# Kernel optimization log

Hardware: AMD Instinct MI355X
Metric: run time of the kernel (lower is better)

## Reference

```python
import jax, jax.numpy as jnp
import numpy as np

N = 10000        # num nodes
E = 160000       # num edges (before self-loops)
D = 128          # input_dim == 4*hidden_dim
H = 4            # heads for first 19 layers
C = 32           # hidden_dim (per-head channels)
L_MID = 19       # layers with relu (convs[0..18]); last layer is heads=1, concat=False
NEG_SLOPE = 0.2  # PyG GATConv default negative_slope
EPS = 1e-16      # PyG softmax epsilon


def setup_inputs() -> dict:
    key = jax.random.key(0)
    ks = jax.random.split(key, 10)
    s = 0.1  # keep activations stable across 20 layers
    x = jax.random.normal(ks[0], (N, D), jnp.float32)
    edge_index = jax.random.randint(ks[1], (2, E), 0, N, dtype=jnp.int64)
    Ws = jax.random.normal(ks[2], (L_MID, D, H * C), jnp.float32) * s
    a_src = jax.random.normal(ks[3], (L_MID, H, C), jnp.float32) * s
    a_dst = jax.random.normal(ks[4], (L_MID, H, C), jnp.float32) * s
    bs = jnp.zeros((L_MID, H * C), jnp.float32)
    W_last = jax.random.normal(ks[5], (D, D), jnp.float32) * s
    a_src_last = jax.random.normal(ks[6], (1, D), jnp.float32) * s
    a_dst_last = jax.random.normal(ks[7], (1, D), jnp.float32) * s
    b_last = jnp.zeros((D,), jnp.float32)
    return {"x": x, "edge_index": edge_index, "Ws": Ws, "a_src": a_src,
            "a_dst": a_dst, "bs": bs, "W_last": W_last,
            "a_src_last": a_src_last, "a_dst_last": a_dst_last, "b_last": b_last}


def _gat_layer(x, src, dst, W, asrc, adst, heads, ch):
    # x: [N, Din]; W: [Din, heads*ch]; asrc/adst: [heads, ch]
    h = (x @ W).reshape(N, heads, ch)                       # [N,H,C]
    es = jnp.einsum('nhc,hc->nh', h, asrc)                  # [N,H]
    ed = jnp.einsum('nhc,hc->nh', h, adst)                  # [N,H]
    e = jax.nn.leaky_relu(es[src] + ed[dst], NEG_SLOPE)     # [Etot,H]
    # segment softmax over incoming edges of each dst node
    m = jax.ops.segment_max(e, dst, num_segments=N)         # [N,H]
    p = jnp.exp(e - m[dst])
    z = jax.ops.segment_sum(p, dst, num_segments=N)         # [N,H]
    alpha = p / (z[dst] + EPS)                              # [Etot,H]
    msg = h[src] * alpha[:, :, None]                        # [Etot,H,C]
    return jax.ops.segment_sum(msg, dst, num_segments=N)    # [N,H,C]


def reference(x, edge_index, Ws, a_src, a_dst, bs, W_last, a_src_last, a_dst_last, b_last):
    # PyG GATConv adds self-loops by default
    loop = jnp.arange(N, dtype=edge_index.dtype)
    src = jnp.concatenate([edge_index[0], loop])
    dst = jnp.concatenate([edge_index[1], loop])

    def mid_step(h, params):
        W, asrc, adst, b = params
        out = _gat_layer(h, src, dst, W, asrc, adst, H, C).reshape(N, H * C) + b
        return jax.nn.relu(out), None  # training dropout omitted (eval mode)

    x, _ = jax.lax.scan(mid_step, x, (Ws, a_src, a_dst, bs))
    # final layer: heads=1, concat=False -> mean over heads, no relu
    out = _gat_layer(x, src, dst, W_last, a_src_last, a_dst_last, 1, D)
    return out.mean(axis=1) + b_last
```

## Files before the change

kernel.cpp:

```cpp
#include <hip/hip_runtime.h>
#include <hip/hip_bf16.h>
#include <math.h>

#define D 128
#define NEG 0.2f
#define EPSV 1e-16f
#define NPB 8
#define GRP_N 4

__global__ void scan_kernel(const int* __restrict__ deg, int N, int* __restrict__ row_ptr, int* __restrict__ cursor){
  __shared__ int part[1024];
  const int CH = 16;
  int t = threadIdx.x;
  int base = t*CH;
  int local[CH]; int s = 0;
  #pragma unroll
  for (int j=0;j<CH;j++){ int idx=base+j; int v = (idx<N)? deg[idx] : 0; local[j]=s; s+=v; }
  part[t]=s; __syncthreads();
  for (int off=1; off<1024; off<<=1){
    int v = (t>=off)? part[t-off] : 0;
    __syncthreads();
    part[t]+=v;
    __syncthreads();
  }
  int cb = (t==0)? 0 : part[t-1];
  #pragma unroll
  for (int j=0;j<CH;j++){ int idx=base+j; if(idx<N){ int r=cb+local[j]; row_ptr[idx]=r; cursor[idx]=r; } }
  if (t==1023) row_ptr[N]=part[1023];
}

__global__ void scatter_kernel(const int* __restrict__ esrc, const int* __restrict__ edst,
                               int E, int N, int* __restrict__ cursor, int* __restrict__ csr_src){
  int i = blockIdx.x*blockDim.x + threadIdx.x;
  int tot = E + N;
  if (i>=tot) return;
  int s, d2;
  if (i<E){ s=esrc[i]; d2=edst[i]; } else { s=i-E; d2=i-E; }
  int pos = atomicAdd(&cursor[d2],1);
  csr_src[pos]=s;
}

template<int HNEXT>
__device__ __forceinline__ void gemv_phase(const float (*rbuf)[D], int nbase, int N,
                                           const float* __restrict__ Wn,
                                           const float* __restrict__ av_, const float* __restrict__ bv_,
                                           float* __restrict__ h_out, float* __restrict__ es_out,
                                           float* __restrict__ ed_out, float (*pE)[2], float (*pD)[2]){
  const int t   = threadIdx.x;
  const int col = t & (D-1);
  const int g   = t >> 7;
  const float av = av_[col], bv = bv_[col];
  const float* __restrict__ r[GRP_N];
  #pragma unroll
  for (int j=0;j<GRP_N;j++) r[j] = rbuf[g*GRP_N + j];
  float acc[GRP_N];
  #pragma unroll
  for (int j=0;j<GRP_N;j++) acc[j]=0.f;

  #pragma unroll 4
  for (int k=0;k<D;k+=4){
    const float w0 = Wn[(size_t)(k+0)*D + col];
    const float w1 = Wn[(size_t)(k+1)*D + col];
    const float w2 = Wn[(size_t)(k+2)*D + col];
    const float w3 = Wn[(size_t)(k+3)*D + col];
    #pragma unroll
    for (int j=0;j<GRP_N;j++){
      const float4 xv = *reinterpret_cast<const float4*>(r[j] + k);
      acc[j] = fmaf(xv.w, w3, fmaf(xv.z, w2, fmaf(xv.y, w1, fmaf(xv.x, w0, acc[j]))));
    }
  }

  if constexpr (HNEXT==4){
    #pragma unroll
    for (int j=0;j<GRP_N;j++){
      const int n = nbase + g*GRP_N + j;
      if (n < N){
        __builtin_nontemporal_store(acc[j], &h_out[(size_t)n*D + col]);
        float ps = acc[j]*av, pd = acc[j]*bv;
        #pragma unroll
        for (int off=16; off; off>>=1){ ps += __shfl_xor(ps, off, 32); pd += __shfl_xor(pd, off, 32); }
        if ((col&31)==0){ es_out[n*4 + (col>>5)] = ps; ed_out[n*4 + (col>>5)] = pd; }
      }
    }
  } else {
    const int half = (t>>6)&1;
    #pragma unroll
    for (int j=0;j<GRP_N;j++){
      const int n = nbase + g*GRP_N + j;
      float ps = 0.f, pd = 0.f;
      if (n < N){
        __builtin_nontemporal_store(acc[j], &h_out[(size_t)n*D + col]);
        ps = acc[j]*av; pd = acc[j]*bv;
      }
      #pragma unroll
      for (int off=32; off; off>>=1){ ps += __shfl_xor(ps, off, 64); pd += __shfl_xor(pd, off, 64); }
      if ((t&63)==0){ pE[g*GRP_N+j][half]=ps; pD[g*GRP_N+j][half]=pd; }
    }
    __syncthreads();
    if (t < NPB){
      const int n = nbase + t;
      if (n < N){
        es_out[n] = pE[t][0]+pE[t][1];
        ed_out[n] = pD[t][0]+pD[t][1];
      }
    }
  }
}

__launch_bounds__(256, 4)
__global__ void linear0_kernel(const float* __restrict__ x, const float* __restrict__ Wn,
                               const float* __restrict__ an_src, const float* __restrict__ an_dst,
                               int N, int E, const int* __restrict__ edst, int* __restrict__ deg,
                               float* __restrict__ h_out, float* __restrict__ es_out, float* __restrict__ ed_out){
  __shared__ float rbuf[NPB][D];
  __shared__ float pE[NPB][2], pD[NPB][2];
  const int t = threadIdx.x;
  const int nbase = blockIdx.x*NPB;
  {
    const int gid = blockIdx.x*256 + t;
    const int gs  = gridDim.x*256;
    const int tot = E + N;
    for (int i = gid; i < tot; i += gs){
      const int d2 = (i < E) ? edst[i] : (i - E);
      atomicAdd(&deg[d2], 1);
    }
  }
  {
    const int row = t >> 5;
    const int cc  = (t & 31) * 4;
    int n = nbase + row; if (n > N-1) n = N-1;
    const float4 v = *reinterpret_cast<const float4*>(x + (size_t)n*D + cc);
    *reinterpret_cast<float4*>(&rbuf[row][cc]) = v;
  }
  __syncthreads();
  gemv_phase<4>(rbuf, nbase, N, Wn, an_src, an_dst, h_out, es_out, ed_out, pE, pD);
}

template<int HNEXT>
__launch_bounds__(256, 4)
__global__ void fused_kernel(const float* __restrict__ h, const float* __restrict__ es, const float* __restrict__ ed,
                             const int* __restrict__ row_ptr, const int* __restrict__ csr_src,
                             const float* __restrict__ bias,
                             const float* __restrict__ Wn, const float* __restrict__ an_src, const float* __restrict__ an_dst,
                             int N, float* __restrict__ h_out, float* __restrict__ es_out, float* __restrict__ ed_out){
  __shared__ int   sIdx[NPB][32];
  __shared__ float sP[NPB][32][4];
  __shared__ float rbuf[NPB][D];
  __shared__ float pE[NPB][2], pD[NPB][2];
  const int t = threadIdx.x;
  const int hw  = t >> 5;
  const int l32 = t & 31;
  const int cq   = l32 * 4;
  const int myh4 = l32 >> 3;
  const int nbase = blockIdx.x*NPB;
  const int n = nbase + hw;

  if (n < N){
    const int start = row_ptr[n], end = row_ptr[n+1];
    const float4 edv = *reinterpret_cast<const float4*>(ed + (size_t)n*4);
    float4 acc = make_float4(0.f,0.f,0.f,0.f);
    float z = 0.f;

    for (int t0 = start; t0 < end; t0 += 32){
      const int cnt = min(32, end - t0);
      {
        int sOff = 0; float p0=0.f,p1=0.f,p2=0.f,p3=0.f;
        if (l32 < cnt){
          const int s = csr_src[t0 + l32];
          sOff = s*D;
          const float4 e4 = *reinterpret_cast<const float4*>(es + (size_t)s*4);
          float q0 = e4.x + edv.x; q0 = (q0>=0.f)? q0 : NEG*q0; q0 = fminf(q0, 80.f);
          float q1 = e4.y + edv.y; q1 = (q1>=0.f)? q1 : NEG*q1; q1 = fminf(q1, 80.f);
          float q2 = e4.z + edv.z; q2 = (q2>=0.f)? q2 : NEG*q2; q2 = fminf(q2, 80.f);
          float q3 = e4.w + edv.w; q3 = (q3>=0.f)? q3 : NEG*q3; q3 = fminf(q3, 80.f);
          p0 = __expf(q0); p1 = __expf(q1); p2 = __expf(q2); p3 = __expf(q3);
        }
        sIdx[hw][l32] = sOff;
        *reinterpret_cast<float4*>(&sP[hw][l32][0]) = make_float4(p0,p1,p2,p3);
      }
      #pragma unroll 8
      for (int e = 0; e < cnt; e++){
        const int   off = sIdx[hw][e];
        const float p   = sP[hw][e][myh4];
        const float4 hv = *reinterpret_cast<const float4*>(h + (size_t)off + cq);
        z += p;
        acc.x = fmaf(p, hv.x, acc.x);
        acc.y = fmaf(p, hv.y, acc.y);
        acc.z = fmaf(p, hv.z, acc.z);
        acc.w = fmaf(p, hv.w, acc.w);
      }
    }
    const float inv = 1.f/(z + EPSV);
    const float4 bv = *reinterpret_cast<const float4*>(bias + cq);
    float4 o;
    o.x = fmaxf(fmaf(acc.x, inv, bv.x), 0.f);
    o.y = fmaxf(fmaf(acc.y, inv, bv.y), 0.f);
    o.z = fmaxf(fmaf(acc.z, inv, bv.z), 0.f);
    o.w = fmaxf(fmaf(acc.w, inv, bv.w), 0.f);
    *reinterpret_cast<float4*>(&rbuf[hw][cq]) = o;
  } else {
    *reinterpret_cast<float4*>(&rbuf[hw][cq]) = make_float4(0.f,0.f,0.f,0.f);
  }
  __syncthreads();
  gemv_phase<HNEXT>(rbuf, nbase, N, Wn, an_src, an_dst, h_out, es_out, ed_out, pE, pD);
}

__launch_bounds__(256, 4)
__global__ void final_agg_kernel(const float* __restrict__ h, const float* __restrict__ es, const float* __restrict__ ed,
                                 const int* __restrict__ row_ptr, const int* __restrict__ csr_src,
                                 const float* __restrict__ bias, float* __restrict__ out, int N){
  __shared__ int   sIdx[NPB][32];
  __shared__ float sP[NPB][32];
  const int t = threadIdx.x;
  const int hw  = t >> 5;
  const int l32 = t & 31;
  const int cq  = l32 * 4;
  const int n = blockIdx.x*NPB + hw;
  if (n >= N) return;
  const int start = row_ptr[n], end = row_ptr[n+1];
  const float edn = ed[n];
  float4 acc = make_float4(0.f,0.f,0.f,0.f);
  float z = 0.f;
  for (int t0 = start; t0 < end; t0 += 32){
    const int cnt = min(32, end - t0);
    {
      int sOff = 0; float p0 = 0.f;
      if (l32 < cnt){
        const int s = csr_src[t0 + l32];
        sOff = s*D;
        float q0 = es[s] + edn; q0 = (q0>=0.f)? q0 : NEG*q0; q0 = fminf(q0, 80.f);
        p0 = __expf(q0);
      }
      sIdx[hw][l32] = sOff;
      sP[hw][l32] = p0;
    }
    #pragma unroll 8
    for (int e = 0; e < cnt; e++){
      const int   off = sIdx[hw][e];
      const float p   = sP[hw][e];
      const float4 hv = *reinterpret_cast<const float4*>(h + (size_t)off + cq);
      z += p;
      acc.x = fmaf(p, hv.x, acc.x);
      acc.y = fmaf(p, hv.y, acc.y);
      acc.z = fmaf(p, hv.z, acc.z);
      acc.w = fmaf(p, hv.w, acc.w);
    }
  }
  const float inv = 1.f/(z + EPSV);
  const float4 bv = *reinterpret_cast<const float4*>(bias + cq);
  float4 o;
  o.x = fmaf(acc.x, inv, bv.x);
  o.y = fmaf(acc.y, inv, bv.y);
  o.z = fmaf(acc.z, inv, bv.z);
  o.w = fmaf(acc.w, inv, bv.w);
  *reinterpret_cast<float4*>(&out[(size_t)n*D + cq]) = o;
}

extern "C" void kernel_launch(void* const* d_in, const int* in_sizes, int n_in,
                              void* d_out, int out_size, void* d_ws, size_t ws_size,
                              hipStream_t stream) {
  const float* x          = (const float*)d_in[0];
  const int*   ei         = (const int*)d_in[1];
  const float* Ws         = (const float*)d_in[2];
  const float* a_src      = (const float*)d_in[3];
  const float* a_dst      = (const float*)d_in[4];
  const float* bs         = (const float*)d_in[5];
  const float* W_last     = (const float*)d_in[6];
  const float* a_src_last = (const float*)d_in[7];
  const float* a_dst_last = (const float*)d_in[8];
  const float* b_last     = (const float*)d_in[9];

  const int N = in_sizes[0]/D;
  const int E = in_sizes[1]/2;
  const int L = in_sizes[2]/(D*D);
  const int* esrc = ei;
  const int* edst = ei + E;

  char* ws = (char*)d_ws;
  float* h0  = (float*)ws;  ws += (size_t)N*D*sizeof(float);
  float* h1  = (float*)ws;  ws += (size_t)N*D*sizeof(float);
  float* es0 = (float*)ws;  ws += (size_t)N*4*sizeof(float);
  float* es1 = (float*)ws;  ws += (size_t)N*4*sizeof(float);
  float* ed0 = (float*)ws;  ws += (size_t)N*4*sizeof(float);
  float* ed1 = (float*)ws;  ws += (size_t)N*4*sizeof(float);
  int* deg     = (int*)ws;  ws += (size_t)N*sizeof(int);
  int* row_ptr = (int*)ws;  ws += (size_t)(N+1)*sizeof(int);
  int* cursor  = (int*)ws;  ws += (size_t)N*sizeof(int);
  int* csr_src = (int*)ws;  ws += (size_t)(E+N)*sizeof(int);

  const int tot = E + N;
  const int gA = (N + NPB - 1)/NPB;

  hipMemsetAsync(deg, 0, (size_t)N*sizeof(int), stream);
  linear0_kernel<<<gA, 256, 0, stream>>>(x, Ws, a_src, a_dst, N, E, edst, deg, h0, es0, ed0);
  scan_kernel<<<1, 1024, 0, stream>>>(deg, N, row_ptr, cursor);
  scatter_kernel<<<(tot+255)/256, 256, 0, stream>>>(esrc, edst, E, N, cursor, csr_src);

  const float *hc = h0, *esc = es0, *edc = ed0;
  float *hn = h1, *esn = es1, *edn = ed1;

  for (int l = 0; l < L-1; l++){
    fused_kernel<4><<<gA, 256, 0, stream>>>(hc, esc, edc, row_ptr, csr_src,
                                            bs + (size_t)l*D,
                                            Ws + (size_t)(l+1)*D*D, a_src + (size_t)(l+1)*D, a_dst + (size_t)(l+1)*D,
                                            N, hn, esn, edn);
    const float* tf;
    tf = hc;  hc = hn;  hn = (float*)tf;
    tf = esc; esc = esn; esn = (float*)tf;
    tf = edc; edc = edn; edn = (float*)tf;
  }

  fused_kernel<1><<<gA, 256, 0, stream>>>(hc, esc, edc, row_ptr, csr_src,
                                          bs + (size_t)(L-1)*D,
                                          W_last, a_src_last, a_dst_last,
                                          N, hn, esn, edn);
  {
    const float* tf;
    tf = hc;  hc = hn;  hn = (float*)tf;
    tf = esc; esc = esn; esn = (float*)tf;
    tf = edc; edc = edn; edn = (float*)tf;
  }

  final_agg_kernel<<<gA, 256, 0, stream>>>(hc, esc, edc, row_ptr, csr_src, b_last, (float*)d_out, N);
}
```

Baseline: 433.4 us.

## Fuse all GAT layers into one persistent kernel with grid-wide barriers

Replaces the per-layer kernel launches (20 fused layers plus final aggregation) with a single persistent kernel of 500 blocks × 512 threads, each owning 20 nodes. A hand-rolled slotted atomic grid barrier separates layers. Cross-block data now goes through relaxed agent-scope atomic loads and stores, split into float2 pieces. The degree count moves back into its own kernel. This aims to remove launch overhead and tail gaps between layers, but it relies on every block being co-resident, since the barrier has a timeout escape. It also gives up vectorized float4 and nontemporal memory accesses.

```diff
diff --git a/kernel.cpp b/kernel.cpp
--- a/kernel.cpp
+++ b/kernel.cpp
@@ -5,8 +5,50 @@
 #define D 128
 #define NEG 0.2f
 #define EPSV 1e-16f
-#define NPB 8
-#define GRP_N 4
+#define NPB 20
+#define GRPN 5
+#define NSYNC 20
+#define BAR_U32 144
+
+__device__ __forceinline__ float2 ld_sys_f2(const float* p){
+  unsigned long long u = __hip_atomic_load((const unsigned long long*)p, __ATOMIC_RELAXED, __HIP_MEMORY_SCOPE_AGENT);
+  float2 f; f.x = __uint_as_float((unsigned)u); f.y = __uint_as_float((unsigned)(u >> 32));
+  return f;
+}
+__device__ __forceinline__ float ld_sys_f1(const float* p){
+  return __uint_as_float(__hip_atomic_load((const unsigned*)p, __ATOMIC_RELAXED, __HIP_MEMORY_SCOPE_AGENT));
+}
+__device__ __forceinline__ void st_sys_f1(float* p, float v){
+  __hip_atomic_store((unsigned*)p, __float_as_uint(v), __ATOMIC_RELAXED, __HIP_MEMORY_SCOPE_AGENT);
+}
+
+__device__ __forceinline__ void gsync(unsigned* bar, int idx){
+  __syncthreads();
+  if (threadIdx.x == 0){
+    unsigned* b = bar + idx * BAR_U32;
+    const unsigned g = gridDim.x;
+    const unsigned nslots = (g < 8u) ? g : 8u;
+    const unsigned slot = blockIdx.x & 7u;
+    const unsigned target = ((g - 1u - slot) >> 3) + 1u;
+    const unsigned a = __hip_atomic_fetch_add(b + slot*16, 1u, __ATOMIC_RELAXED, __HIP_MEMORY_SCOPE_AGENT);
+    if (a == target - 1u)
+      __hip_atomic_fetch_add(b + 128, 1u, __ATOMIC_RELAXED, __HIP_MEMORY_SCOPE_AGENT);
+    int fuse = 0;
+    while (__hip_atomic_load(b + 128, __ATOMIC_RELAXED, __HIP_MEMORY_SCOPE_AGENT) < nslots){
+      __builtin_amdgcn_s_sleep(2);
+      if (++fuse > (1<<22)) break;
+    }
+  }
+  __syncthreads();
+}
+
+__global__ void count_kernel(const int* __restrict__ edst, int E, int N, int* __restrict__ deg){
+  int i = blockIdx.x*blockDim.x + threadIdx.x;
+  int tot = E + N;
+  if (i >= tot) return;
+  int d = (i < E) ? edst[i] : (i - E);
+  atomicAdd(&deg[d], 1);
+}
 
 __global__ void scan_kernel(const int* __restrict__ deg, int N, int* __restrict__ row_ptr, int* __restrict__ cursor){
   __shared__ int part[1024];
@@ -44,18 +86,18 @@
 __device__ __forceinline__ void gemv_phase(const float (*rbuf)[D], int nbase, int N,
                                            const float* __restrict__ Wn,
                                            const float* __restrict__ av_, const float* __restrict__ bv_,
-                                           float* __restrict__ h_out, float* __restrict__ es_out,
-                                           float* __restrict__ ed_out, float (*pE)[2], float (*pD)[2]){
+                                           float* h_out, float* es_out, float* ed_out,
+                                           float (*pE)[2], float (*pD)[2]){
   const int t   = threadIdx.x;
   const int col = t & (D-1);
   const int g   = t >> 7;
   const float av = av_[col], bv = bv_[col];
-  const float* __restrict__ r[GRP_N];
+  const float* __restrict__ r[GRPN];
   #pragma unroll
-  for (int j=0;j<GRP_N;j++) r[j] = rbuf[g*GRP_N + j];
-  float acc[GRP_N];
+  for (int j=0;j<GRPN;j++) r[j] = rbuf[g*GRPN + j];
+  float acc[GRPN];
   #pragma unroll
-  for (int j=0;j<GRP_N;j++) acc[j]=0.f;
+  for (int j=0;j<GRPN;j++) acc[j]=0.f;
 
   #pragma unroll 4
   for (int k=0;k<D;k+=4){
@@ -64,7 +106,7 @@
     const float w2 = Wn[(size_t)(k+2)*D + col];
     const float w3 = Wn[(size_t)(k+3)*D + col];
     #pragma unroll
-    for (int j=0;j<GRP_N;j++){
+    for (int j=0;j<GRPN;j++){
       const float4 xv = *reinterpret_cast<const float4*>(r[j] + k);
       acc[j] = fmaf(xv.w, w3, fmaf(xv.z, w2, fmaf(xv.y, w1, fmaf(xv.x, w0, acc[j]))));
     }
@@ -72,95 +114,57 @@
 
   if constexpr (HNEXT==4){
     #pragma unroll
-    for (int j=0;j<GRP_N;j++){
-      const int n = nbase + g*GRP_N + j;
+    for (int j=0;j<GRPN;j++){
+      const int n = nbase + g*GRPN + j;
       if (n < N){
-        __builtin_nontemporal_store(acc[j], &h_out[(size_t)n*D + col]);
+        st_sys_f1(&h_out[(size_t)n*D + col], acc[j]);
         float ps = acc[j]*av, pd = acc[j]*bv;
         #pragma unroll
         for (int off=16; off; off>>=1){ ps += __shfl_xor(ps, off, 32); pd += __shfl_xor(pd, off, 32); }
-        if ((col&31)==0){ es_out[n*4 + (col>>5)] = ps; ed_out[n*4 + (col>>5)] = pd; }
+        if ((col&31)==0){ st_sys_f1(&es_out[n*4 + (col>>5)], ps); st_sys_f1(&ed_out[n*4 + (col>>5)], pd); }
       }
     }
   } else {
     const int half = (t>>6)&1;
     #pragma unroll
-    for (int j=0;j<GRP_N;j++){
-      const int n = nbase + g*GRP_N + j;
+    for (int j=0;j<GRPN;j++){
+      const int n = nbase + g*GRPN + j;
       float ps = 0.f, pd = 0.f;
       if (n < N){
-        __builtin_nontemporal_store(acc[j], &h_out[(size_t)n*D + col]);
+        st_sys_f1(&h_out[(size_t)n*D + col], acc[j]);
         ps = acc[j]*av; pd = acc[j]*bv;
       }
       #pragma unroll
       for (int off=32; off; off>>=1){ ps += __shfl_xor(ps, off, 64); pd += __shfl_xor(pd, off, 64); }
-      if ((t&63)==0){ pE[g*GRP_N+j][half]=ps; pD[g*GRP_N+j][half]=pd; }
+      if ((t&63)==0){ pE[g*GRPN+j][half]=ps; pD[g*GRPN+j][half]=pd; }
     }
     __syncthreads();
     if (t < NPB){
       const int n = nbase + t;
       if (n < N){
-        es_out[n] = pE[t][0]+pE[t][1];
-        ed_out[n] = pD[t][0]+pD[t][1];
-      }
-    }
-  }
-}
-
-__launch_bounds__(256, 4)
-__global__ void linear0_kernel(const float* __restrict__ x, const float* __restrict__ Wn,
-                               const float* __restrict__ an_src, const float* __restrict__ an_dst,
-                               int N, int E, const int* __restrict__ edst, int* __restrict__ deg,
-                               float* __restrict__ h_out, float* __restrict__ es_out, float* __restrict__ ed_out){
-  __shared__ float rbuf[NPB][D];
-  __shared__ float pE[NPB][2], pD[NPB][2];
+        st_sys_f1(&es_out[n], pE[t][0]+pE[t][1]);
+        st_sys_f1(&ed_out[n], pD[t][0]+pD[t][1]);
+      }
+    }
+  }
+}
+
+__device__ __forceinline__ void mid_agg(const float* h, const float* es, const float* ed,
+                                        const int* __restrict__ row_ptr, const int* __restrict__ csr_src,
+                                        const float* __restrict__ bias,
+                                        float (*rbuf)[D], int (*sIdx)[32], float (*sP)[32][4],
+                                        int nbase, int N){
   const int t = threadIdx.x;
-  const int nbase = blockIdx.x*NPB;
-  {
-    const int gid = blockIdx.x*256 + t;
-    const int gs  = gridDim.x*256;
-    const int tot = E + N;
-    for (int i = gid; i < tot; i += gs){
-      const int d2 = (i < E) ? edst[i] : (i - E);
-      atomicAdd(&deg[d2], 1);
-    }
-  }
-  {
-    const int row = t >> 5;
-    const int cc  = (t & 31) * 4;
-    int n = nbase + row; if (n > N-1) n = N-1;
-    const float4 v = *reinterpret_cast<const float4*>(x + (size_t)n*D + cc);
-    *reinterpret_cast<float4*>(&rbuf[row][cc]) = v;
-  }
-  __syncthreads();
-  gemv_phase<4>(rbuf, nbase, N, Wn, an_src, an_dst, h_out, es_out, ed_out, pE, pD);
-}
-
-template<int HNEXT>
-__launch_bounds__(256, 4)
-__global__ void fused_kernel(const float* __restrict__ h, const float* __restrict__ es, const float* __restrict__ ed,
-                             const int* __restrict__ row_ptr, const int* __restrict__ csr_src,
-                             const float* __restrict__ bias,
-                             const float* __restrict__ Wn, const float* __restrict__ an_src, const float* __restrict__ an_dst,
-                             int N, float* __restrict__ h_out, float* __restrict__ es_out, float* __restrict__ ed_out){
-  __shared__ int   sIdx[NPB][32];
-  __shared__ float sP[NPB][32][4];
-  __shared__ float rbuf[NPB][D];
-  __shared__ float pE[NPB][2], pD[NPB][2];
-  const int t = threadIdx.x;
-  const int hw  = t >> 5;
-  const int l32 = t & 31;
-  const int cq   = l32 * 4;
-  const int myh4 = l32 >> 3;
-  const int nbase = blockIdx.x*NPB;
-  const int n = nbase + hw;
-
-  if (n < N){
+  const int hw = t >> 5, l32 = t & 31;
+  const int cq = l32*4, myh4 = l32>>3;
+  for (int local = hw; local < NPB; local += 16){
+    const int n = nbase + local;
+    if (n >= N){ *reinterpret_cast<float4*>(&rbuf[local][cq]) = make_float4(0.f,0.f,0.f,0.f); continue; }
     const int start = row_ptr[n], end = row_ptr[n+1];
-    const float4 edv = *reinterpret_cast<const float4*>(ed + (size_t)n*4);
+    const float2 edA = ld_sys_f2(ed + (size_t)n*4);
+    const float2 edB = ld_sys_f2(ed + (size_t)n*4 + 2);
     float4 acc = make_float4(0.f,0.f,0.f,0.f);
     float z = 0.f;
-
     for (int t0 = start; t0 < end; t0 += 32){
       const int cnt = min(32, end - t0);
       {
@@ -168,11 +172,12 @@
         if (l32 < cnt){
           const int s = csr_src[t0 + l32];
           sOff = s*D;
-          const float4 e4 = *reinterpret_cast<const float4*>(es + (size_t)s*4);
-          float q0 = e4.x + edv.x; q0 = (q0>=0.f)? q0 : NEG*q0; q0 = fminf(q0, 80.f);
-          float q1 = e4.y + edv.y; q1 = (q1>=0.f)? q1 : NEG*q1; q1 = fminf(q1, 80.f);
-          float q2 = e4.z + edv.z; q2 = (q2>=0.f)? q2 : NEG*q2; q2 = fminf(q2, 80.f);
-          float q3 = e4.w + edv.w; q3 = (q3>=0.f)? q3 : NEG*q3; q3 = fminf(q3, 80.f);
+          const float2 eA = ld_sys_f2(es + (size_t)s*4);
+          const float2 eB = ld_sys_f2(es + (size_t)s*4 + 2);
+          float q0 = eA.x + edA.x; q0 = (q0>=0.f)? q0 : NEG*q0; q0 = fminf(q0, 80.f);
+          float q1 = eA.y + edA.y; q1 = (q1>=0.f)? q1 : NEG*q1; q1 = fminf(q1, 80.f);
+          float q2 = eB.x + edB.x; q2 = (q2>=0.f)? q2 : NEG*q2; q2 = fminf(q2, 80.f);
+          float q3 = eB.y + edB.y; q3 = (q3>=0.f)? q3 : NEG*q3; q3 = fminf(q3, 80.f);
           p0 = __expf(q0); p1 = __expf(q1); p2 = __expf(q2); p3 = __expf(q3);
         }
         sIdx[hw][l32] = sOff;
@@ -182,12 +187,13 @@
       for (int e = 0; e < cnt; e++){
         const int   off = sIdx[hw][e];
         const float p   = sP[hw][e][myh4];
-        const float4 hv = *reinterpret_cast<const float4*>(h + (size_t)off + cq);
+        const float2 hA = ld_sys_f2(h + (size_t)off + cq);
+        const float2 hB = ld_sys_f2(h + (size_t)off + cq + 2);
         z += p;
-        acc.x = fmaf(p, hv.x, acc.x);
-        acc.y = fmaf(p, hv.y, acc.y);
-        acc.z = fmaf(p, hv.z, acc.z);
-        acc.w = fmaf(p, hv.w, acc.w);
+        acc.x = fmaf(p, hA.x, acc.x);
+        acc.y = fmaf(p, hA.y, acc.y);
+        acc.z = fmaf(p, hB.x, acc.z);
+        acc.w = fmaf(p, hB.y, acc.w);
       }
     }
     const float inv = 1.f/(z + EPSV);
@@ -197,63 +203,115 @@
     o.y = fmaxf(fmaf(acc.y, inv, bv.y), 0.f);
     o.z = fmaxf(fmaf(acc.z, inv, bv.z), 0.f);
     o.w = fmaxf(fmaf(acc.w, inv, bv.w), 0.f);
-    *reinterpret_cast<float4*>(&rbuf[hw][cq]) = o;
-  } else {
-    *reinterpret_cast<float4*>(&rbuf[hw][cq]) = make_float4(0.f,0.f,0.f,0.f);
+    *reinterpret_cast<float4*>(&rbuf[local][cq]) = o;
+  }
+}
+
+__device__ __forceinline__ void final_agg(const float* h, const float* es, const float* ed,
+                                          const int* __restrict__ row_ptr, const int* __restrict__ csr_src,
+                                          const float* __restrict__ bias, float* __restrict__ out,
+                                          int (*sIdx)[32], float (*sP)[32][4], int nbase, int N){
+  const int t = threadIdx.x;
+  const int hw = t >> 5, l32 = t & 31;
+  const int cq = l32*4;
+  for (int local = hw; local < NPB; local += 16){
+    const int n = nbase + local;
+    if (n >= N) continue;
+    const int start = row_ptr[n], end = row_ptr[n+1];
+    const float edn = ld_sys_f1(ed + n);
+    float4 acc = make_float4(0.f,0.f,0.f,0.f);
+    float z = 0.f;
+    for (int t0 = start; t0 < end; t0 += 32){
+      const int cnt = min(32, end - t0);
+      {
+        int sOff = 0; float p0 = 0.f;
+        if (l32 < cnt){
+          const int s = csr_src[t0 + l32];
+          sOff = s*D;
+          float q0 = ld_sys_f1(es + s) + edn; q0 = (q0>=0.f)? q0 : NEG*q0; q0 = fminf(q0, 80.f);
+          p0 = __expf(q0);
+        }
+        sIdx[hw][l32] = sOff;
+        sP[hw][l32][0] = p0;
+      }
+      #pragma unroll 8
+      for (int e = 0; e < cnt; e++){
+        const int   off = sIdx[hw][e];
+        const float p   = sP[hw][e][0];
+        const float2 hA = ld_sys_f2(h + (size_t)off + cq);
+        const float2 hB = ld_sys_f2(h + (size_t)off + cq + 2);
+        z += p;
+        acc.x = fmaf(p, hA.x, acc.x);
+        acc.y = fmaf(p, hA.y, acc.y);
+        acc.z = fmaf(p, hB.x, acc.z);
+        acc.w = fmaf(p, hB.y, acc.w);
+      }
+    }
+    const float inv = 1.f/(z + EPSV);
+    const float4 bv = *reinterpret_cast<const float4*>(bias + cq);
+    float4 o;
+    o.x = fmaf(acc.x, inv, bv.x);
+    o.y = fmaf(acc.y, inv, bv.y);
+    o.z = fmaf(acc.z, inv, bv.z);
+    o.w = fmaf(acc.w, inv, bv.w);
+    *reinterpret_cast<float4*>(&out[(size_t)n*D + cq]) = o;
+  }
+}
+
+__global__ __launch_bounds__(512, 4)
+void gat_persist(const float* __restrict__ x,
+                 const int* __restrict__ row_ptr, const int* __restrict__ csr_src,
+                 const float* __restrict__ Ws, const float* __restrict__ a_src, const float* __restrict__ a_dst,
+                 const float* __restrict__ bs, const float* __restrict__ W_last,
+                 const float* __restrict__ a_src_last, const float* __restrict__ a_dst_last,
+                 const float* __restrict__ b_last,
+                 int N, int L,
+                 float* h0, float* h1, float* es0, float* es1, float* ed0, float* ed1,
+                 unsigned* bar, float* out){
+  __shared__ float rbuf[NPB][D];
+  __shared__ int   sIdx[16][32];
+  __shared__ float sP[16][32][4];
+  __shared__ float pE[NPB][2], pD[NPB][2];
+  const int t = threadIdx.x;
+  const int nbase = blockIdx.x * NPB;
+  int sync_idx = 0;
+
+  for (int i = t; i < NPB*(D/4); i += 512){
+    const int row = i >> 5;
+    const int cc  = (i & 31) * 4;
+    int n = nbase + row; if (n > N-1) n = N-1;
+    *reinterpret_cast<float4*>(&rbuf[row][cc]) = *reinterpret_cast<const float4*>(x + (size_t)n*D + cc);
   }
   __syncthreads();
-  gemv_phase<HNEXT>(rbuf, nbase, N, Wn, an_src, an_dst, h_out, es_out, ed_out, pE, pD);
-}
-
-__launch_bounds__(256, 4)
-__global__ void final_agg_kernel(const float* __restrict__ h, const float* __restrict__ es, const float* __restrict__ ed,
-                                 const int* __restrict__ row_ptr, const int* __restrict__ csr_src,
-                                 const float* __restrict__ bias, float* __restrict__ out, int N){
-  __shared__ int   sIdx[NPB][32];
-  __shared__ float sP[NPB][32];
-  const int t = threadIdx.x;
-  const int hw  = t >> 5;
-  const int l32 = t & 31;
-  const int cq  = l32 * 4;
-  const int n = blockIdx.x*NPB + hw;
-  if (n >= N) return;
-  const int start = row_ptr[n], end = row_ptr[n+1];
-  const float edn = ed[n];
-  float4 acc = make_float4(0.f,0.f,0.f,0.f);
-  float z = 0.f;
-  for (int t0 = start; t0 < end; t0 += 32){
-    const int cnt = min(32, end - t0);
-    {
-      int sOff = 0; float p0 = 0.f;
-      if (l32 < cnt){
-        const int s = csr_src[t0 + l32];
-        sOff = s*D;
-        float q0 = es[s] + edn; q0 = (q0>=0.f)? q0 : NEG*q0; q0 = fminf(q0, 80.f);
-        p0 = __expf(q0);
-      }
-      sIdx[hw][l32] = sOff;
-      sP[hw][l32] = p0;
-    }
-    #pragma unroll 8
-    for (int e = 0; e < cnt; e++){
-      const int   off = sIdx[hw][e];
-      const float p   = sP[hw][e];
-      const float4 hv = *reinterpret_cast<const float4*>(h + (size_t)off + cq);
-      z += p;
-      acc.x = fmaf(p, hv.x, acc.x);
-      acc.y = fmaf(p, hv.y, acc.y);
-      acc.z = fmaf(p, hv.z, acc.z);
-      acc.w = fmaf(p, hv.w, acc.w);
-    }
-  }
-  const float inv = 1.f/(z + EPSV);
-  const float4 bv = *reinterpret_cast<const float4*>(bias + cq);
-  float4 o;
-  o.x = fmaf(acc.x, inv, bv.x);
-  o.y = fmaf(acc.y, inv, bv.y);
-  o.z = fmaf(acc.z, inv, bv.z);
-  o.w = fmaf(acc.w, inv, bv.w);
-  *reinterpret_cast<float4*>(&out[(size_t)n*D + cq]) = o;
+  float *hc = h0, *esc = es0, *edc = ed0;
+  float *hn = h1, *esn = es1, *edn = ed1;
+  gemv_phase<4>(rbuf, nbase, N, Ws, a_src, a_dst, hc, esc, edc, pE, pD);
+  gsync(bar, sync_idx++);
+
+  for (int l = 0; l < L-1; ++l){
+    mid_agg(hc, esc, edc, row_ptr, csr_src, bs + (size_t)l*D, rbuf, sIdx, sP, nbase, N);
+    __syncthreads();
+    gemv_phase<4>(rbuf, nbase, N, Ws + (size_t)(l+1)*D*D, a_src + (size_t)(l+1)*D, a_dst + (size_t)(l+1)*D,
+                  hn, esn, edn, pE, pD);
+    gsync(bar, sync_idx++);
+    float* tp;
+    tp = hc;  hc = hn;  hn = tp;
+    tp = esc; esc = esn; esn = tp;
+    tp = edc; edc = edn; edn = tp;
+  }
+
+  mid_agg(hc, esc, edc, row_ptr, csr_src, bs + (size_t)(L-1)*D, rbuf, sIdx, sP, nbase, N);
+  __syncthreads();
+  gemv_phase<1>(rbuf, nbase, N, W_last, a_src_last, a_dst_last, hn, esn, edn, pE, pD);
+  gsync(bar, sync_idx++);
+  {
+    float* tp;
+    tp = hc;  hc = hn;  hn = tp;
+    tp = esc; esc = esn; esn = tp;
+    tp = edc; edc = edn; edn = tp;
+  }
+
+  final_agg(hc, esc, edc, row_ptr, csr_src, b_last, out, sIdx, sP, nbase, N);
 }
 
 extern "C" void kernel_launch(void* const* d_in, const int* in_sizes, int n_in,
@@ -277,49 +335,30 @@
   const int* edst = ei + E;
 
   char* ws = (char*)d_ws;
+  int* deg       = (int*)ws;      ws += (size_t)N*sizeof(int);
+  unsigned* bar  = (unsigned*)ws; ws += (size_t)NSYNC*BAR_U32*sizeof(unsigned);
+  int* row_ptr = (int*)ws;  ws += (size_t)(N+1)*sizeof(int);
+  int* cursor  = (int*)ws;  ws += (size_t)N*sizeof(int);
+  int* csr_src = (int*)ws;  ws += (size_t)(E+N)*sizeof(int);
   float* h0  = (float*)ws;  ws += (size_t)N*D*sizeof(float);
   float* h1  = (float*)ws;  ws += (size_t)N*D*sizeof(float);
   float* es0 = (float*)ws;  ws += (size_t)N*4*sizeof(float);
   float* es1 = (float*)ws;  ws += (size_t)N*4*sizeof(float);
   float* ed0 = (float*)ws;  ws += (size_t)N*4*sizeof(float);
   float* ed1 = (float*)ws;  ws += (size_t)N*4*sizeof(float);
-  int* deg     = (int*)ws;  ws += (size_t)N*sizeof(int);
-  int* row_ptr = (int*)ws;  ws += (size_t)(N+1)*sizeof(int);
-  int* cursor  = (int*)ws;  ws += (size_t)N*sizeof(int);
-  int* csr_src = (int*)ws;  ws += (size_t)(E+N)*sizeof(int);
 
   const int tot = E + N;
   const int gA = (N + NPB - 1)/NPB;
 
-  hipMemsetAsync(deg, 0, (size_t)N*sizeof(int), stream);
-  linear0_kernel<<<gA, 256, 0, stream>>>(x, Ws, a_src, a_dst, N, E, edst, deg, h0, es0, ed0);
+  hipMemsetAsync(deg, 0, (size_t)N*sizeof(int) + (size_t)NSYNC*BAR_U32*sizeof(unsigned), stream);
+  count_kernel<<<(tot+255)/256, 256, 0, stream>>>(edst, E, N, deg);
   scan_kernel<<<1, 1024, 0, stream>>>(deg, N, row_ptr, cursor);
   scatter_kernel<<<(tot+255)/256, 256, 0, stream>>>(esrc, edst, E, N, cursor, csr_src);
 
-  const float *hc = h0, *esc = es0, *edc = ed0;
-  float *hn = h1, *esn = es1, *edn = ed1;
-
-  for (int l = 0; l < L-1; l++){
-    fused_kernel<4><<<gA, 256, 0, stream>>>(hc, esc, edc, row_ptr, csr_src,
-                                            bs + (size_t)l*D,
-                                            Ws + (size_t)(l+1)*D*D, a_src + (size_t)(l+1)*D, a_dst + (size_t)(l+1)*D,
-                                            N, hn, esn, edn);
-    const float* tf;
-    tf = hc;  hc = hn;  hn = (float*)tf;
-    tf = esc; esc = esn; esn = (float*)tf;
-    tf = edc; edc = edn; edn = (float*)tf;
-  }
-
-  fused_kernel<1><<<gA, 256, 0, stream>>>(hc, esc, edc, row_ptr, csr_src,
-                                          bs + (size_t)(L-1)*D,
-                                          W_last, a_src_last, a_dst_last,
-                                          N, hn, esn, edn);
-  {
-    const float* tf;
-    tf = hc;  hc = hn;  hn = (float*)tf;
-    tf = esc; esc = esn; esn = (float*)tf;
-    tf = edc; edc = edn; edn = (float*)tf;
-  }
-
-  final_agg_kernel<<<gA, 256, 0, stream>>>(hc, esc, edc, row_ptr, csr_src, b_last, (float*)d_out, N);
-}
+  gat_persist<<<gA, 512, 0, stream>>>(x, row_ptr, csr_src,
+                                      Ws, a_src, a_dst, bs,
+                                      W_last, a_src_last, a_dst_last, b_last,
+                                      N, L,
+                                      h0, h1, es0, es1, ed0, ed1,
+                                      bar, (float*)d_out);
+}
```

Result: slower. 619.8 us (+43.0%).

## Fold degree count into single-block CSR prep and scatter into linear0

Applied to the files above, without the earlier changes.

Degree counting moves into a single-block kernel that histograms in shared memory and scans it. The CSR scatter moves into linear0, which removes the memset and the separate scatter launch. The aggregation loop is also unrolled by two with dual accumulators to expose more memory-level parallelism. The single block does all 160k atomics serially on one CU, which could cost more than the removed launches. Shared memory is capped at MAXN nodes.

```diff
diff --git a/kernel.cpp b/kernel.cpp
--- a/kernel.cpp
+++ b/kernel.cpp
@@ -7,37 +7,34 @@
 #define EPSV 1e-16f
 #define NPB 8
 #define GRP_N 4
-
-__global__ void scan_kernel(const int* __restrict__ deg, int N, int* __restrict__ row_ptr, int* __restrict__ cursor){
+#define MAXN 10240
+
+__global__ __launch_bounds__(1024, 1)
+void csrprep_kernel(const int* __restrict__ edst, int E, int N,
+                    int* __restrict__ row_ptr, int* __restrict__ cursor){
+  __shared__ int ldeg[MAXN];
   __shared__ int part[1024];
-  const int CH = 16;
-  int t = threadIdx.x;
-  int base = t*CH;
+  const int t = threadIdx.x;
+  for (int i = t; i < N; i += 1024) ldeg[i] = 0;
+  __syncthreads();
+  for (int i = t; i < E; i += 1024) atomicAdd(&ldeg[edst[i]], 1);
+  __syncthreads();
+  const int CH = MAXN/1024;
+  const int base = t*CH;
   int local[CH]; int s = 0;
   #pragma unroll
-  for (int j=0;j<CH;j++){ int idx=base+j; int v = (idx<N)? deg[idx] : 0; local[j]=s; s+=v; }
+  for (int j=0;j<CH;j++){ const int idx=base+j; const int v=(idx<N)? (ldeg[idx]+1) : 0; local[j]=s; s+=v; }
   part[t]=s; __syncthreads();
   for (int off=1; off<1024; off<<=1){
-    int v = (t>=off)? part[t-off] : 0;
+    const int v = (t>=off)? part[t-off] : 0;
     __syncthreads();
     part[t]+=v;
     __syncthreads();
   }
-  int cb = (t==0)? 0 : part[t-1];
+  const int cb = (t==0)? 0 : part[t-1];
   #pragma unroll
-  for (int j=0;j<CH;j++){ int idx=base+j; if(idx<N){ int r=cb+local[j]; row_ptr[idx]=r; cursor[idx]=r; } }
+  for (int j=0;j<CH;j++){ const int idx=base+j; if(idx<N){ const int r=cb+local[j]; row_ptr[idx]=r; cursor[idx]=r; } }
   if (t==1023) row_ptr[N]=part[1023];
-}
-
-__global__ void scatter_kernel(const int* __restrict__ esrc, const int* __restrict__ edst,
-                               int E, int N, int* __restrict__ cursor, int* __restrict__ csr_src){
-  int i = blockIdx.x*blockDim.x + threadIdx.x;
-  int tot = E + N;
-  if (i>=tot) return;
-  int s, d2;
-  if (i<E){ s=esrc[i]; d2=edst[i]; } else { s=i-E; d2=i-E; }
-  int pos = atomicAdd(&cursor[d2],1);
-  csr_src[pos]=s;
 }
 
 template<int HNEXT>
@@ -110,7 +107,8 @@
 __launch_bounds__(256, 4)
 __global__ void linear0_kernel(const float* __restrict__ x, const float* __restrict__ Wn,
                                const float* __restrict__ an_src, const float* __restrict__ an_dst,
-                               int N, int E, const int* __restrict__ edst, int* __restrict__ deg,
+                               int N, int E, const int* __restrict__ esrc, const int* __restrict__ edst,
+                               int* __restrict__ cursor, int* __restrict__ csr_src,
                                float* __restrict__ h_out, float* __restrict__ es_out, float* __restrict__ ed_out){
   __shared__ float rbuf[NPB][D];
   __shared__ float pE[NPB][2], pD[NPB][2];
@@ -121,8 +119,10 @@
     const int gs  = gridDim.x*256;
     const int tot = E + N;
     for (int i = gid; i < tot; i += gs){
-      const int d2 = (i < E) ? edst[i] : (i - E);
-      atomicAdd(&deg[d2], 1);
+      int s2, d2;
+      if (i < E){ s2 = esrc[i]; d2 = edst[i]; } else { s2 = i - E; d2 = i - E; }
+      const int pos = atomicAdd(&cursor[d2], 1);
+      csr_src[pos] = s2;
     }
   }
   {
@@ -158,8 +158,9 @@
   if (n < N){
     const int start = row_ptr[n], end = row_ptr[n+1];
     const float4 edv = *reinterpret_cast<const float4*>(ed + (size_t)n*4);
-    float4 acc = make_float4(0.f,0.f,0.f,0.f);
-    float z = 0.f;
+    float4 a0 = make_float4(0.f,0.f,0.f,0.f);
+    float4 a1 = make_float4(0.f,0.f,0.f,0.f);
+    float z0 = 0.f, z1 = 0.f;
 
     for (int t0 = start; t0 < end; t0 += 32){
       const int cnt = min(32, end - t0);
@@ -178,18 +179,34 @@
         sIdx[hw][l32] = sOff;
         *reinterpret_cast<float4*>(&sP[hw][l32][0]) = make_float4(p0,p1,p2,p3);
       }
-      #pragma unroll 8
-      for (int e = 0; e < cnt; e++){
+      int e = 0;
+      #pragma unroll 4
+      for (; e+2 <= cnt; e += 2){
+        const int   off0 = sIdx[hw][e];
+        const int   off1 = sIdx[hw][e+1];
+        const float p0   = sP[hw][e][myh4];
+        const float p1   = sP[hw][e+1][myh4];
+        const float4 hv0 = *reinterpret_cast<const float4*>(h + (size_t)off0 + cq);
+        const float4 hv1 = *reinterpret_cast<const float4*>(h + (size_t)off1 + cq);
+        z0 += p0; z1 += p1;
+        a0.x = fmaf(p0, hv0.x, a0.x); a1.x = fmaf(p1, hv1.x, a1.x);
+        a0.y = fmaf(p0, hv0.y, a0.y); a1.y = fmaf(p1, hv1.y, a1.y);
+        a0.z = fmaf(p0, hv0.z, a0.z); a1.z = fmaf(p1, hv1.z, a1.z);
+        a0.w = fmaf(p0, hv0.w, a0.w); a1.w = fmaf(p1, hv1.w, a1.w);
+      }
+      if (e < cnt){
         const int   off = sIdx[hw][e];
         const float p   = sP[hw][e][myh4];
         const float4 hv = *reinterpret_cast<const float4*>(h + (size_t)off + cq);
-        z += p;
-        acc.x = fmaf(p, hv.x, acc.x);
-        acc.y = fmaf(p, hv.y, acc.y);
-        acc.z = fmaf(p, hv.z, acc.z);
-        acc.w = fmaf(p, hv.w, acc.w);
-      }
-    }
+        z0 += p;
+        a0.x = fmaf(p, hv.x, a0.x);
+        a0.y = fmaf(p, hv.y, a0.y);
+        a0.z = fmaf(p, hv.z, a0.z);
+        a0.w = fmaf(p, hv.w, a0.w);
+      }
+    }
+    const float z = z0 + z1;
+    const float4 acc = make_float4(a0.x+a1.x, a0.y+a1.y, a0.z+a1.z, a0.w+a1.w);
     const float inv = 1.f/(z + EPSV);
     const float4 bv = *reinterpret_cast<const float4*>(bias + cq);
     float4 o;
@@ -283,18 +300,15 @@
   float* es1 = (float*)ws;  ws += (size_t)N*4*sizeof(float);
   float* ed0 = (float*)ws;  ws += (size_t)N*4*sizeof(float);
   float* ed1 = (float*)ws;  ws += (size_t)N*4*sizeof(float);
-  int* deg     = (int*)ws;  ws += (size_t)N*sizeof(int);
   int* row_ptr = (int*)ws;  ws += (size_t)(N+1)*sizeof(int);
   int* cursor  = (int*)ws;  ws += (size_t)N*sizeof(int);
   int* csr_src = (int*)ws;  ws += (size_t)(E+N)*sizeof(int);
 
-  const int tot = E + N;
   const int gA = (N + NPB - 1)/NPB;
 
-  hipMemsetAsync(deg, 0, (size_t)N*sizeof(int), stream);
-  linear0_kernel<<<gA, 256, 0, stream>>>(x, Ws, a_src, a_dst, N, E, edst, deg, h0, es0, ed0);
-  scan_kernel<<<1, 1024, 0, stream>>>(deg, N, row_ptr, cursor);
-  scatter_kernel<<<(tot+255)/256, 256, 0, stream>>>(esrc, edst, E, N, cursor, csr_src);
+  csrprep_kernel<<<1, 1024, 0, stream>>>(edst, E, N, row_ptr, cursor);
+  linear0_kernel<<<gA, 256, 0, stream>>>(x, Ws, a_src, a_dst, N, E, esrc, edst,
+                                         cursor, csr_src, h0, es0, ed0);
 
   const float *hc = h0, *esc = es0, *edc = ed0;
   float *hn = h1, *esn = es1, *edn = ed1;
```

Measured after the change: 442.7 us. 2.1% more time.
